# Performance work log

Hardware: AMD Instinct MI355X
Metric: run time of the kernel (lower is better)

The kernel has to match this reference:

```python
import jax, jax.numpy as jnp
import numpy as np

N_NODES = 100000
N_EDGES = 1250000
NUM_RELS = 8
D_IN, D_HID, D_OUT = 64, 64, 32


def setup_inputs() -> dict:
    key = jax.random.key(0)
    ks = jax.random.split(key, 10)
    x = jax.random.normal(ks[0], (N_NODES, D_IN), dtype=jnp.float32)
    src = jax.random.randint(ks[1], (N_EDGES,), 0, N_NODES, dtype=jnp.int32)
    dst = jax.random.randint(ks[2], (N_EDGES,), 0, N_NODES, dtype=jnp.int32)
    edge_type = jax.random.randint(ks[3], (N_EDGES,), 0, NUM_RELS, dtype=jnp.int32)
    s1 = 1.0 / np.sqrt(D_IN)
    s2 = 1.0 / np.sqrt(D_HID)
    W1 = jax.random.uniform(ks[4], (NUM_RELS, D_IN, D_HID), jnp.float32, -s1, s1)
    root1 = jax.random.uniform(ks[5], (D_IN, D_HID), jnp.float32, -s1, s1)
    b1 = jnp.zeros((D_HID,), jnp.float32)
    W2 = jax.random.uniform(ks[6], (NUM_RELS, D_HID, D_OUT), jnp.float32, -s2, s2)
    root2 = jax.random.uniform(ks[7], (D_HID, D_OUT), jnp.float32, -s2, s2)
    b2 = jnp.zeros((D_OUT,), jnp.float32)
    return {"x": x, "W1": W1, "root1": root1, "b1": b1,
            "W2": W2, "root2": root2, "b2": b2,
            "src": src, "dst": dst, "edge_type": edge_type}


def rgcn_conv(x, W, root, b, src, dst, edge_type, num_rels, num_nodes):
    # self-loop (root) transform + bias
    out = x @ root + b
    for r in range(num_rels):  # loop over small fixed relation set
        mask = (edge_type == r).astype(x.dtype)          # (E,)
        h = x @ W[r]                                      # (N, dout): transform once per relation
        msg = h[src] * mask[:, None]                      # (E, dout) gather + mask
        agg = jax.ops.segment_sum(msg, dst, num_segments=num_nodes)
        cnt = jax.ops.segment_sum(mask, dst, num_segments=num_nodes)
        out = out + agg / jnp.maximum(cnt, 1.0)[:, None]  # per-relation mean (PyG default aggr)
    return out


def reference(x, W1, root1, b1, W2, root2, b2, src, dst, edge_type):
    h = jax.nn.relu(rgcn_conv(x, W1, root1, b1, src, dst, edge_type, NUM_RELS, N_NODES))
    return rgcn_conv(h, W2, root2, b2, src, dst, edge_type, NUM_RELS, N_NODES)
```

## Files before the change

kernel.cpp:

```cpp
#include <hip/hip_runtime.h>

typedef _Float16 half8 __attribute__((ext_vector_type(8)));
typedef __attribute__((ext_vector_type(4))) float f32x4;

__device__ __forceinline__ unsigned short f2h(float f) {
    _Float16 h = (_Float16)f;
    return *(unsigned short*)&h;
}
__device__ __forceinline__ float h2f(unsigned short u) {
    _Float16 h = *(_Float16*)&u;
    return (float)h;
}


__global__ __launch_bounds__(256) void hist8_kernel(
    const int* __restrict__ dst, const int* __restrict__ et,
    int* __restrict__ hist, int* __restrict__ rank, int E)
{
    int e = blockIdx.x * 256 + threadIdx.x;
    if (e < E) rank[e] = atomicAdd(&hist[dst[e] * 8 + et[e]], 1);
}

#define SCAN_TILE 4096
__global__ __launch_bounds__(1024) void scanA_kernel(
    const int* __restrict__ hist, int* __restrict__ bstart,
    int* __restrict__ partial, int nkeys)
{
    __shared__ int wsum[16];
    const int t = threadIdx.x;
    const int lane = t & 63, w = t >> 6;
    const int base = blockIdx.x * SCAN_TILE + t * 4;
    int v[4];
    int s = 0;
#pragma unroll
    for (int i = 0; i < 4; ++i) {
        v[i] = (base + i < nkeys) ? hist[base + i] : 0;
        s += v[i];
    }
    int inc = s;
#pragma unroll
    for (int off = 1; off < 64; off <<= 1) {
        int u = __shfl_up(inc, off);
        if (lane >= off) inc += u;
    }
    if (lane == 63) wsum[w] = inc;
    __syncthreads();
    if (w == 0 && lane < 16) {
        int ws = wsum[lane];
        int winc = ws;
#pragma unroll
        for (int off = 1; off < 16; off <<= 1) {
            int u = __shfl_up(winc, off);
            if (lane >= off) winc += u;
        }
        wsum[lane] = winc - ws;
    }
    __syncthreads();
    int run = wsum[w] + (inc - s);
    int tbase = run;
#pragma unroll
    for (int i = 0; i < 4; ++i) {
        if (base + i < nkeys) bstart[base + i] = run;
        run += v[i];
    }
    if (t == 1023) partial[blockIdx.x] = tbase + s;
}

__global__ __launch_bounds__(64) void scanB_kernel(
    const int* __restrict__ partial, int* __restrict__ pscan,
    int* __restrict__ bstart_end, int nblk)
{
    const int lane = threadIdx.x;
    int running = 0;
    for (int b = 0; b < nblk; b += 64) {
        int i = b + lane;
        int o = (i < nblk) ? partial[i] : 0;
        int v = o;
#pragma unroll
        for (int off = 1; off < 64; off <<= 1) {
            int u = __shfl_up(v, off);
            if (lane >= off) v += u;
        }
        if (i < nblk) pscan[i] = running + v - o;
        running += __shfl(v, 63);
    }
    if (lane == 0) *bstart_end = running;
}

__global__ __launch_bounds__(1024) void scanC_kernel(
    int* __restrict__ bstart, const int* __restrict__ pscan, int nkeys)
{
    int i = blockIdx.x * 1024 + threadIdx.x;
    if (i < nkeys) bstart[i] += pscan[i / SCAN_TILE];
}

__global__ __launch_bounds__(256) void scatter9_kernel(
    const int* __restrict__ src, const int* __restrict__ dst,
    const int* __restrict__ et, const int* __restrict__ rank,
    const int* __restrict__ bstart, uint2* __restrict__ srt, int E)
{
    int e = blockIdx.x * 256 + threadIdx.x;
    if (e < E) {
        int r = et[e];
        int key = dst[e] * 8 + r;
        int b0 = bstart[key];
        int cnt = bstart[key + 1] - b0;
        float scale = 1.0f / (float)cnt;
        uint2 rec;
        rec.x = (unsigned)(src[e] * 9 + r);
        rec.y = __float_as_uint(scale);
        srt[b0 + rank[e]] = rec;
    }
}


__global__ __launch_bounds__(256) void wprep9_kernel(
    const float* __restrict__ W, const float* __restrict__ root,
    unsigned short* __restrict__ wb, int dout)
{
    int idx = blockIdx.x * 256 + threadIdx.x;
    int total = 9 * dout * 64;
    if (idx >= total) return;
    int j = idx >> 6;
    int k = idx & 63;
    int c = j / dout, jj = j % dout;
    float f = (c == 0) ? root[k * dout + jj]
                       : W[(size_t)(c - 1) * 64 * dout + k * dout + jj];
    wb[(size_t)j * 72 + k] = f2h(f);
}


template <int AF32>
__global__ __launch_bounds__(512, 2) void gemm9_kernel(
    const void* __restrict__ Av,
    const unsigned short* __restrict__ wb,
    unsigned short* __restrict__ T,
    int trowstride, int n_nodes)
{
    constexpr int NC = 288;
    constexpr int WSH = NC * 72;
    __shared__ __align__(16) unsigned short wt_s[WSH];

    const int t = threadIdx.x;
    const int w = t >> 6, lane = t & 63;
    const int quad = lane >> 4, l16 = lane & 15;
    const int colbase = blockIdx.y * NC;
    const int node0 = blockIdx.x * 128;
    const int row = min(node0 + w * 16 + l16, n_nodes - 1);

    half8 a0, a1;
    if (AF32) {
        const float* ar = (const float*)Av + (size_t)row * 64;
        f32x4 x0 = *(const f32x4*)(ar + quad * 8);
        f32x4 x1 = *(const f32x4*)(ar + quad * 8 + 4);
        f32x4 x2 = *(const f32x4*)(ar + 32 + quad * 8);
        f32x4 x3 = *(const f32x4*)(ar + 32 + quad * 8 + 4);
#pragma unroll
        for (int i = 0; i < 4; ++i) {
            a0[i] = (_Float16)x0[i]; a0[i + 4] = (_Float16)x1[i];
            a1[i] = (_Float16)x2[i]; a1[i + 4] = (_Float16)x3[i];
        }
    } else {
        const unsigned short* ar = (const unsigned short*)Av + (size_t)row * 64;
        a0 = *(const half8*)(ar + quad * 8);
        a1 = *(const half8*)(ar + 32 + quad * 8);
    }

    {
        const uint4* s4 = (const uint4*)(wb + (size_t)colbase * 72);
        uint4* d4 = (uint4*)wt_s;
        for (int i = t; i < WSH / 8; i += 512) d4[i] = s4[i];
    }
    __syncthreads();

    f32x4 d[18];
#pragma unroll
    for (int i = 0; i < 18; ++i) d[i] = {0.f, 0.f, 0.f, 0.f};

#pragma unroll
    for (int jj = 0; jj < 18; ++jj) {
        const int j = jj * 16 + l16;
        half8 b0 = *(const half8*)&wt_s[j * 72 + quad * 8];
        half8 b1 = *(const half8*)&wt_s[j * 72 + 32 + quad * 8];
        d[jj] = __builtin_amdgcn_mfma_f32_16x16x32_f16(a0, b0, d[jj], 0, 0, 0);
        d[jj] = __builtin_amdgcn_mfma_f32_16x16x32_f16(a1, b1, d[jj], 0, 0, 0);
    }

#pragma unroll
    for (int jj = 0; jj < 18; ++jj) {
#pragma unroll
        for (int r = 0; r < 4; ++r) {
            const int node = node0 + w * 16 + quad * 4 + r;
            if (node < n_nodes)
                T[(size_t)node * trowstride + colbase + jj * 16 + l16] = f2h(d[jj][r]);
        }
    }
}


template <int DHALF, int RELU>
__global__ __launch_bounds__(512) void aggT_kernel(
    const unsigned short* __restrict__ T,
    const uint2* __restrict__ srt,
    const int* __restrict__ bstart,
    const float* __restrict__ bias,
    unsigned short* __restrict__ outh,
    float* __restrict__ outf,
    int n_nodes)
{
    constexpr int SUB = 64 / DHALF;
    const int t = threadIdx.x;
    const int lane = t & 63;
    const int node = blockIdx.x * 8 + (t >> 6);
    if (node >= n_nodes) return;
    const int lf = lane & (DHALF - 1);
    const int sub = (SUB == 2) ? (lane >> 5) : 0;

    const int e0 = bstart[node * 8];
    const int e1 = bstart[node * 8 + 8];

    float acc0 = 0.f, acc1 = 0.f;
    for (int base = e0; base < e1; base += 64) {
        const int blen = min(64, e1 - base);
        uint2 rec; rec.x = 0u; rec.y = 0u;
        if (lane < blen) rec = srt[base + lane];
        int k = 0;
        for (; k + 4 * SUB <= blen; k += 4 * SUB) {
            const int i0 = k + sub;
            const int i1 = k + SUB + sub;
            const int i2 = k + 2 * SUB + sub;
            const int i3 = k + 3 * SUB + sub;
            unsigned q0 = __shfl(rec.x, i0), q1 = __shfl(rec.x, i1);
            unsigned q2 = __shfl(rec.x, i2), q3 = __shfl(rec.x, i3);
            float s0 = __uint_as_float(__shfl(rec.y, i0));
            float s1 = __uint_as_float(__shfl(rec.y, i1));
            float s2 = __uint_as_float(__shfl(rec.y, i2));
            float s3 = __uint_as_float(__shfl(rec.y, i3));
            float v0 = h2f(T[(size_t)(q0 + 1) * DHALF + lf]);
            float v1 = h2f(T[(size_t)(q1 + 1) * DHALF + lf]);
            float v2 = h2f(T[(size_t)(q2 + 1) * DHALF + lf]);
            float v3 = h2f(T[(size_t)(q3 + 1) * DHALF + lf]);
            acc0 = fmaf(v0, s0, acc0);
            acc1 = fmaf(v1, s1, acc1);
            acc0 = fmaf(v2, s2, acc0);
            acc1 = fmaf(v3, s3, acc1);
        }
        for (; k < blen; k += SUB) {
            const int idx = k + sub;
            unsigned q = __shfl(rec.x, idx);
            float s = __uint_as_float(__shfl(rec.y, idx));
            if (SUB == 2 && idx >= blen) s = 0.f;
            float v = h2f(T[(size_t)(q + 1) * DHALF + lf]);
            acc0 = fmaf(v, s, acc0);
        }
    }
    float acc = acc0 + acc1;
    if (SUB == 2) acc += __shfl_xor(acc, 32);

    float o = h2f(T[(size_t)node * (9 * DHALF) + lf]) + bias[lf] + acc;
    if (RELU) o = fmaxf(o, 0.f);
    if (DHALF == 64) {
        outh[(size_t)node * 64 + lane] = f2h(o);
    } else if (lane < 32) {
        outf[(size_t)node * 32 + lane] = o;
    }
}

extern "C" void kernel_launch(void* const* d_in, const int* in_sizes, int n_in,
                              void* d_out, int out_size, void* d_ws, size_t ws_size,
                              hipStream_t stream) {
    const float* x     = (const float*)d_in[0];
    const float* W1    = (const float*)d_in[1];
    const float* root1 = (const float*)d_in[2];
    const float* b1    = (const float*)d_in[3];
    const float* W2    = (const float*)d_in[4];
    const float* root2 = (const float*)d_in[5];
    const float* b2    = (const float*)d_in[6];
    const int*   src   = (const int*)d_in[7];
    const int*   dst   = (const int*)d_in[8];
    const int*   et    = (const int*)d_in[9];

    const int N = in_sizes[0] / 64;
    const int E = in_sizes[7];
    const int KEYS = N * 8;

    char* p = (char*)d_ws;
    auto alloc = [&](size_t bytes) {
        char* r = p;
        p += (bytes + 15) & ~(size_t)15;
        return r;
    };
    uint2* srt          = (uint2*)alloc((size_t)E * 8);
    int* rank           = (int*)alloc((size_t)E * 4);
    int* hist           = (int*)alloc((size_t)KEYS * 4);
    int* bstart         = (int*)alloc((size_t)(KEYS + 1) * 4);
    int* partial        = (int*)alloc(256 * 4);
    int* pscan          = (int*)alloc(256 * 4);
    unsigned short* wb1 = (unsigned short*)alloc((size_t)576 * 72 * 2);
    unsigned short* wb2 = (unsigned short*)alloc((size_t)288 * 72 * 2);
    unsigned short* T   = (unsigned short*)alloc((size_t)N * 576 * 2);
    unsigned short* h   = (unsigned short*)alloc((size_t)N * 64 * 2);

    hipMemsetAsync(hist, 0, (size_t)KEYS * 4, stream);
    wprep9_kernel<<<(576 * 64 + 255) / 256, 256, 0, stream>>>(W1, root1, wb1, 64);
    wprep9_kernel<<<(288 * 64 + 255) / 256, 256, 0, stream>>>(W2, root2, wb2, 32);
    hist8_kernel<<<(E + 255) / 256, 256, 0, stream>>>(dst, et, hist, rank, E);
    const int nscan = (KEYS + SCAN_TILE - 1) / SCAN_TILE;
    scanA_kernel<<<nscan, 1024, 0, stream>>>(hist, bstart, partial, KEYS);
    scanB_kernel<<<1, 64, 0, stream>>>(partial, pscan, bstart + KEYS, nscan);
    scanC_kernel<<<(KEYS + 1023) / 1024, 1024, 0, stream>>>(bstart, pscan, KEYS);
    scatter9_kernel<<<(E + 255) / 256, 256, 0, stream>>>(src, dst, et, rank, bstart, srt, E);

    gemm9_kernel<1><<<dim3((N + 127) / 128, 2), 512, 0, stream>>>(x, wb1, T, 576, N);
    aggT_kernel<64, 1><<<(N + 7) / 8, 512, 0, stream>>>(T, srt, bstart, b1, h, nullptr, N);
    gemm9_kernel<0><<<dim3((N + 127) / 128, 1), 512, 0, stream>>>(h, wb2, T, 288, N);
    aggT_kernel<32, 0><<<(N + 7) / 8, 512, 0, stream>>>(T, srt, bstart, b2, nullptr,
                                                        (float*)d_out, N);
}
```

Before: 353.4 us.

## Aggregate raw features per relation before dense transform instead of transforming first

```diff
diff --git a/kernel.cpp b/kernel.cpp
--- a/kernel.cpp
+++ b/kernel.cpp
@@ -10,6 +10,23 @@
 __device__ __forceinline__ float h2f(unsigned short u) {
     _Float16 h = *(_Float16*)&u;
     return (float)h;
+}
+
+
+__global__ __launch_bounds__(256) void xprep_kernel(
+    const float* __restrict__ x, unsigned short* __restrict__ xh, int total8)
+{
+    int i = blockIdx.x * 256 + threadIdx.x;
+    if (i >= total8) return;
+    const f32x4* p = (const f32x4*)(x + (size_t)i * 8);
+    f32x4 u = p[0], v = p[1];
+    half8 o;
+#pragma unroll
+    for (int j = 0; j < 4; ++j) {
+        o[j] = (_Float16)u[j];
+        o[j + 4] = (_Float16)v[j];
+    }
+    *(half8*)(xh + (size_t)i * 8) = o;
 }
 
 
@@ -94,175 +111,164 @@
     if (i < nkeys) bstart[i] += pscan[i / SCAN_TILE];
 }
 
-__global__ __launch_bounds__(256) void scatter9_kernel(
+__global__ __launch_bounds__(256) void scatter_kernel(
     const int* __restrict__ src, const int* __restrict__ dst,
     const int* __restrict__ et, const int* __restrict__ rank,
-    const int* __restrict__ bstart, uint2* __restrict__ srt, int E)
+    const int* __restrict__ bstart, unsigned* __restrict__ srt, int E)
 {
     int e = blockIdx.x * 256 + threadIdx.x;
     if (e < E) {
-        int r = et[e];
-        int key = dst[e] * 8 + r;
-        int b0 = bstart[key];
-        int cnt = bstart[key + 1] - b0;
-        float scale = 1.0f / (float)cnt;
-        uint2 rec;
-        rec.x = (unsigned)(src[e] * 9 + r);
-        rec.y = __float_as_uint(scale);
-        srt[b0 + rank[e]] = rec;
-    }
-}
-
-
-__global__ __launch_bounds__(256) void wprep9_kernel(
+        int key = dst[e] * 8 + et[e];
+        srt[bstart[key] + rank[e]] = (unsigned)src[e];
+    }
+}
+
+
+__global__ __launch_bounds__(256) void wprep_kernel(
     const float* __restrict__ W, const float* __restrict__ root,
     unsigned short* __restrict__ wb, int dout)
 {
     int idx = blockIdx.x * 256 + threadIdx.x;
-    int total = 9 * dout * 64;
+    int total = 9 * 64 * dout;
     if (idx >= total) return;
-    int j = idx >> 6;
-    int k = idx & 63;
-    int c = j / dout, jj = j % dout;
-    float f = (c == 0) ? root[k * dout + jj]
-                       : W[(size_t)(c - 1) * 64 * dout + k * dout + jj];
-    wb[(size_t)j * 72 + k] = f2h(f);
-}
-
-
-template <int AF32>
-__global__ __launch_bounds__(512, 2) void gemm9_kernel(
-    const void* __restrict__ Av,
-    const unsigned short* __restrict__ wb,
-    unsigned short* __restrict__ T,
-    int trowstride, int n_nodes)
-{
-    constexpr int NC = 288;
-    constexpr int WSH = NC * 72;
-    __shared__ __align__(16) unsigned short wt_s[WSH];
-
-    const int t = threadIdx.x;
-    const int w = t >> 6, lane = t & 63;
-    const int quad = lane >> 4, l16 = lane & 15;
-    const int colbase = blockIdx.y * NC;
-    const int node0 = blockIdx.x * 128;
-    const int row = min(node0 + w * 16 + l16, n_nodes - 1);
-
-    half8 a0, a1;
-    if (AF32) {
-        const float* ar = (const float*)Av + (size_t)row * 64;
-        f32x4 x0 = *(const f32x4*)(ar + quad * 8);
-        f32x4 x1 = *(const f32x4*)(ar + quad * 8 + 4);
-        f32x4 x2 = *(const f32x4*)(ar + 32 + quad * 8);
-        f32x4 x3 = *(const f32x4*)(ar + 32 + quad * 8 + 4);
-#pragma unroll
-        for (int i = 0; i < 4; ++i) {
-            a0[i] = (_Float16)x0[i]; a0[i + 4] = (_Float16)x1[i];
-            a1[i] = (_Float16)x2[i]; a1[i + 4] = (_Float16)x3[i];
-        }
-    } else {
-        const unsigned short* ar = (const unsigned short*)Av + (size_t)row * 64;
-        a0 = *(const half8*)(ar + quad * 8);
-        a1 = *(const half8*)(ar + 32 + quad * 8);
-    }
-
-    {
-        const uint4* s4 = (const uint4*)(wb + (size_t)colbase * 72);
-        uint4* d4 = (uint4*)wt_s;
-        for (int i = t; i < WSH / 8; i += 512) d4[i] = s4[i];
-    }
-    __syncthreads();
-
-    f32x4 d[18];
-#pragma unroll
-    for (int i = 0; i < 18; ++i) d[i] = {0.f, 0.f, 0.f, 0.f};
-
-#pragma unroll
-    for (int jj = 0; jj < 18; ++jj) {
-        const int j = jj * 16 + l16;
-        half8 b0 = *(const half8*)&wt_s[j * 72 + quad * 8];
-        half8 b1 = *(const half8*)&wt_s[j * 72 + 32 + quad * 8];
-        d[jj] = __builtin_amdgcn_mfma_f32_16x16x32_f16(a0, b0, d[jj], 0, 0, 0);
-        d[jj] = __builtin_amdgcn_mfma_f32_16x16x32_f16(a1, b1, d[jj], 0, 0, 0);
-    }
-
-#pragma unroll
-    for (int jj = 0; jj < 18; ++jj) {
-#pragma unroll
-        for (int r = 0; r < 4; ++r) {
-            const int node = node0 + w * 16 + quad * 4 + r;
-            if (node < n_nodes)
-                T[(size_t)node * trowstride + colbase + jj * 16 + l16] = f2h(d[jj][r]);
-        }
-    }
-}
-
-
-template <int DHALF, int RELU>
-__global__ __launch_bounds__(512) void aggT_kernel(
-    const unsigned short* __restrict__ T,
-    const uint2* __restrict__ srt,
+    int c = idx / (64 * dout);
+    int rme = idx % (64 * dout);
+    int kk = rme / dout;
+    int j = rme % dout;
+    float f = (c == 0) ? root[kk * dout + j]
+                       : W[(size_t)(c - 1) * 64 * dout + kk * dout + j];
+    wb[(size_t)c * dout * 72 + (size_t)j * 72 + kk] = f2h(f);
+}
+
+
+__global__ __launch_bounds__(512) void aggM_kernel(
+    const unsigned short* __restrict__ tab,
+    const unsigned* __restrict__ srt,
     const int* __restrict__ bstart,
-    const float* __restrict__ bias,
-    unsigned short* __restrict__ outh,
-    float* __restrict__ outf,
+    unsigned short* __restrict__ M,
     int n_nodes)
 {
-    constexpr int SUB = 64 / DHALF;
     const int t = threadIdx.x;
     const int lane = t & 63;
     const int node = blockIdx.x * 8 + (t >> 6);
     if (node >= n_nodes) return;
-    const int lf = lane & (DHALF - 1);
-    const int sub = (SUB == 2) ? (lane >> 5) : 0;
-
-    const int e0 = bstart[node * 8];
-    const int e1 = bstart[node * 8 + 8];
-
-    float acc0 = 0.f, acc1 = 0.f;
+    int myb = 0;
+    if (lane < 9) myb = bstart[node * 8 + lane];
+    const int e0 = __shfl(myb, 0);
+    const int e1 = __shfl(myb, 8);
+    unsigned short* mrow = M + (size_t)node * 512;
+
+    int r = 0;
+    int bprev = e0;
+    int bnext = __shfl(myb, 1);
+    float acc = 0.f;
+
+    auto flush_to = [&](int eabs) {
+        while (r < 8 && eabs == bnext) {
+            int cnt = bnext - bprev;
+            mrow[r * 64 + lane] = f2h(acc * (cnt ? (1.0f / (float)cnt) : 0.0f));
+            acc = 0.f;
+            bprev = bnext;
+            ++r;
+            bnext = (r < 8) ? __shfl(myb, r + 1) : (e1 + 1);
+        }
+    };
+
     for (int base = e0; base < e1; base += 64) {
         const int blen = min(64, e1 - base);
-        uint2 rec; rec.x = 0u; rec.y = 0u;
+        unsigned rec = 0;
         if (lane < blen) rec = srt[base + lane];
         int k = 0;
-        for (; k + 4 * SUB <= blen; k += 4 * SUB) {
-            const int i0 = k + sub;
-            const int i1 = k + SUB + sub;
-            const int i2 = k + 2 * SUB + sub;
-            const int i3 = k + 3 * SUB + sub;
-            unsigned q0 = __shfl(rec.x, i0), q1 = __shfl(rec.x, i1);
-            unsigned q2 = __shfl(rec.x, i2), q3 = __shfl(rec.x, i3);
-            float s0 = __uint_as_float(__shfl(rec.y, i0));
-            float s1 = __uint_as_float(__shfl(rec.y, i1));
-            float s2 = __uint_as_float(__shfl(rec.y, i2));
-            float s3 = __uint_as_float(__shfl(rec.y, i3));
-            float v0 = h2f(T[(size_t)(q0 + 1) * DHALF + lf]);
-            float v1 = h2f(T[(size_t)(q1 + 1) * DHALF + lf]);
-            float v2 = h2f(T[(size_t)(q2 + 1) * DHALF + lf]);
-            float v3 = h2f(T[(size_t)(q3 + 1) * DHALF + lf]);
-            acc0 = fmaf(v0, s0, acc0);
-            acc1 = fmaf(v1, s1, acc1);
-            acc0 = fmaf(v2, s2, acc0);
-            acc1 = fmaf(v3, s3, acc1);
-        }
-        for (; k < blen; k += SUB) {
-            const int idx = k + sub;
-            unsigned q = __shfl(rec.x, idx);
-            float s = __uint_as_float(__shfl(rec.y, idx));
-            if (SUB == 2 && idx >= blen) s = 0.f;
-            float v = h2f(T[(size_t)(q + 1) * DHALF + lf]);
-            acc0 = fmaf(v, s, acc0);
-        }
-    }
-    float acc = acc0 + acc1;
-    if (SUB == 2) acc += __shfl_xor(acc, 32);
-
-    float o = h2f(T[(size_t)node * (9 * DHALF) + lf]) + bias[lf] + acc;
-    if (RELU) o = fmaxf(o, 0.f);
-    if (DHALF == 64) {
-        outh[(size_t)node * 64 + lane] = f2h(o);
-    } else if (lane < 32) {
-        outf[(size_t)node * 32 + lane] = o;
+        for (; k + 4 <= blen; k += 4) {
+            unsigned q0 = __shfl(rec, k), q1 = __shfl(rec, k + 1);
+            unsigned q2 = __shfl(rec, k + 2), q3 = __shfl(rec, k + 3);
+            float v0 = h2f(tab[(size_t)q0 * 64 + lane]);
+            float v1 = h2f(tab[(size_t)q1 * 64 + lane]);
+            float v2 = h2f(tab[(size_t)q2 * 64 + lane]);
+            float v3 = h2f(tab[(size_t)q3 * 64 + lane]);
+            flush_to(base + k);     acc += v0;
+            flush_to(base + k + 1); acc += v1;
+            flush_to(base + k + 2); acc += v2;
+            flush_to(base + k + 3); acc += v3;
+        }
+        for (; k < blen; ++k) {
+            unsigned q = __shfl(rec, k);
+            float v = h2f(tab[(size_t)q * 64 + lane]);
+            flush_to(base + k);
+            acc += v;
+        }
+    }
+    flush_to(e1);
+}
+
+
+template <int DOUT, int RELU, int OUTH>
+__global__ __launch_bounds__(512, 2) void dense_kernel(
+    const unsigned short* __restrict__ X,
+    const unsigned short* __restrict__ M,
+    const unsigned short* __restrict__ wb,
+    const float* __restrict__ bias,
+    float* __restrict__ outf,
+    unsigned short* __restrict__ outh,
+    int n_nodes)
+{
+    constexpr int WSHORTS = 9 * DOUT * 72;
+    __shared__ __align__(16) unsigned short wt_s[WSHORTS];
+
+    const int t = threadIdx.x;
+    const int w = t >> 6, lane = t & 63;
+    const int quad = lane >> 4, l16 = lane & 15;
+    const int node0 = blockIdx.x * 128;
+    const int row = min(node0 + w * 16 + l16, n_nodes - 1);
+    const unsigned short* xrow = X + (size_t)row * 64;
+    const unsigned short* mrow = M + (size_t)row * 512;
+
+    half8 a[18];
+    a[0] = *(const half8*)(xrow + quad * 8);
+    a[1] = *(const half8*)(xrow + 32 + quad * 8);
+#pragma unroll
+    for (int c = 1; c < 9; ++c) {
+        a[2 * c]     = *(const half8*)(mrow + (c - 1) * 64 + quad * 8);
+        a[2 * c + 1] = *(const half8*)(mrow + (c - 1) * 64 + 32 + quad * 8);
+    }
+    {
+        uint4* d4 = (uint4*)wt_s;
+        const uint4* s4 = (const uint4*)wb;
+        for (int i = t; i < WSHORTS / 8; i += 512) d4[i] = s4[i];
+    }
+    __syncthreads();
+
+    constexpr int JPW = DOUT / 16;
+    f32x4 d[JPW];
+#pragma unroll
+    for (int i = 0; i < JPW; ++i) d[i] = {0.f, 0.f, 0.f, 0.f};
+
+#pragma unroll
+    for (int c = 0; c < 9; ++c) {
+#pragma unroll
+        for (int jj = 0; jj < JPW; ++jj) {
+            const int j = jj * 16 + l16;
+            half8 b0 = *(const half8*)&wt_s[c * DOUT * 72 + j * 72 + quad * 8];
+            half8 b1 = *(const half8*)&wt_s[c * DOUT * 72 + j * 72 + 32 + quad * 8];
+            d[jj] = __builtin_amdgcn_mfma_f32_16x16x32_f16(a[2 * c], b0, d[jj], 0, 0, 0);
+            d[jj] = __builtin_amdgcn_mfma_f32_16x16x32_f16(a[2 * c + 1], b1, d[jj], 0, 0, 0);
+        }
+    }
+
+#pragma unroll
+    for (int jj = 0; jj < JPW; ++jj) {
+        const int j = jj * 16 + l16;
+        const float bj = bias[j];
+#pragma unroll
+        for (int r = 0; r < 4; ++r) {
+            const int node = node0 + w * 16 + quad * 4 + r;
+            if (node < n_nodes) {
+                float v = d[jj][r] + bj;
+                if (RELU) v = fmaxf(v, 0.0f);
+                if (OUTH) outh[(size_t)node * 64 + j] = f2h(v);
+                else      outf[(size_t)node * DOUT + j] = v;
+            }
+        }
     }
 }
 
@@ -290,30 +296,33 @@
         p += (bytes + 15) & ~(size_t)15;
         return r;
     };
-    uint2* srt          = (uint2*)alloc((size_t)E * 8);
+    unsigned* srt       = (unsigned*)alloc((size_t)E * 4);
     int* rank           = (int*)alloc((size_t)E * 4);
     int* hist           = (int*)alloc((size_t)KEYS * 4);
     int* bstart         = (int*)alloc((size_t)(KEYS + 1) * 4);
     int* partial        = (int*)alloc(256 * 4);
     int* pscan          = (int*)alloc(256 * 4);
-    unsigned short* wb1 = (unsigned short*)alloc((size_t)576 * 72 * 2);
-    unsigned short* wb2 = (unsigned short*)alloc((size_t)288 * 72 * 2);
-    unsigned short* T   = (unsigned short*)alloc((size_t)N * 576 * 2);
+    unsigned short* wb1 = (unsigned short*)alloc((size_t)9 * 64 * 72 * 2);
+    unsigned short* wb2 = (unsigned short*)alloc((size_t)9 * 32 * 72 * 2);
+    unsigned short* xh  = (unsigned short*)alloc((size_t)N * 64 * 2);
     unsigned short* h   = (unsigned short*)alloc((size_t)N * 64 * 2);
+    unsigned short* M   = (unsigned short*)alloc((size_t)N * 512 * 2);
 
     hipMemsetAsync(hist, 0, (size_t)KEYS * 4, stream);
-    wprep9_kernel<<<(576 * 64 + 255) / 256, 256, 0, stream>>>(W1, root1, wb1, 64);
-    wprep9_kernel<<<(288 * 64 + 255) / 256, 256, 0, stream>>>(W2, root2, wb2, 32);
+    xprep_kernel<<<(N * 8 + 255) / 256, 256, 0, stream>>>(x, xh, N * 8);
+    wprep_kernel<<<(9 * 64 * 64 + 255) / 256, 256, 0, stream>>>(W1, root1, wb1, 64);
+    wprep_kernel<<<(9 * 64 * 32 + 255) / 256, 256, 0, stream>>>(W2, root2, wb2, 32);
     hist8_kernel<<<(E + 255) / 256, 256, 0, stream>>>(dst, et, hist, rank, E);
     const int nscan = (KEYS + SCAN_TILE - 1) / SCAN_TILE;
     scanA_kernel<<<nscan, 1024, 0, stream>>>(hist, bstart, partial, KEYS);
     scanB_kernel<<<1, 64, 0, stream>>>(partial, pscan, bstart + KEYS, nscan);
     scanC_kernel<<<(KEYS + 1023) / 1024, 1024, 0, stream>>>(bstart, pscan, KEYS);
-    scatter9_kernel<<<(E + 255) / 256, 256, 0, stream>>>(src, dst, et, rank, bstart, srt, E);
-
-    gemm9_kernel<1><<<dim3((N + 127) / 128, 2), 512, 0, stream>>>(x, wb1, T, 576, N);
-    aggT_kernel<64, 1><<<(N + 7) / 8, 512, 0, stream>>>(T, srt, bstart, b1, h, nullptr, N);
-    gemm9_kernel<0><<<dim3((N + 127) / 128, 1), 512, 0, stream>>>(h, wb2, T, 288, N);
-    aggT_kernel<32, 0><<<(N + 7) / 8, 512, 0, stream>>>(T, srt, bstart, b2, nullptr,
-                                                        (float*)d_out, N);
-}
+    scatter_kernel<<<(E + 255) / 256, 256, 0, stream>>>(src, dst, et, rank, bstart, srt, E);
+
+    aggM_kernel<<<(N + 7) / 8, 512, 0, stream>>>(xh, srt, bstart, M, N);
+    dense_kernel<64, 1, 1><<<(N + 127) / 128, 512, 0, stream>>>(
+        xh, M, wb1, b1, nullptr, h, N);
+    aggM_kernel<<<(N + 7) / 8, 512, 0, stream>>>(h, srt, bstart, M, N);
+    dense_kernel<32, 0, 0><<<(N + 127) / 128, 512, 0, stream>>>(
+        h, M, wb2, b2, (float*)d_out, nullptr, N);
+}
```

Result: slower. 408.0 us (+15.4%).
